# Kernel optimization log

Measured on AMD Instinct MI355X. Metric: run time of the kernel, lower is better.

Reference implementation:

```python
import jax, jax.numpy as jnp
import numpy as np

N_NODES = 2000
N_EDGES = 8000  # undirected; 2*N_EDGES directed pairs
BATCH = 16
D = 64  # in/out node and edge feature dim


def _build_graph():
    """Random undirected graph; returns directed (src, dst) pairs in the
    row-major order of torch.where(adj==1), plus the undirected edge id of
    each directed pair (mimics get_all_edge_for_node_pairs)."""
    rng = np.random.default_rng(0)
    cand = rng.integers(0, N_NODES, size=(6 * N_EDGES, 2))
    cand = cand[cand[:, 0] != cand[:, 1]]
    cand = np.sort(cand, axis=1)
    cand = np.unique(cand, axis=0)
    und = cand[:N_EDGES]  # [E,2] unique undirected edges
    adj = np.zeros((N_NODES, N_NODES), dtype=np.int64)
    eid = np.full((N_NODES, N_NODES), -1, dtype=np.int64)
    e = np.arange(N_EDGES)
    adj[und[:, 0], und[:, 1]] = 1
    adj[und[:, 1], und[:, 0]] = 1
    eid[und[:, 0], und[:, 1]] = e
    eid[und[:, 1], und[:, 0]] = e
    src, dst = np.nonzero(adj)  # row-major, like torch.where
    edge_idx = eid[src, dst]
    return src.astype(np.int32), dst.astype(np.int32), edge_idx.astype(np.int32)


def setup_inputs() -> dict:
    key = jax.random.key(0)
    ks = jax.random.split(key, 7)
    src, dst, eidx = _build_graph()
    s = 0.05
    return {
        "x": jax.random.normal(ks[0], (BATCH, N_EDGES + N_NODES, D), jnp.float32),
        "W_edge": jax.random.normal(ks[1], (D, D), jnp.float32) * s,
        "W_node": jax.random.normal(ks[2], (D, D), jnp.float32) * s,
        "b_node": jax.random.normal(ks[3], (D,), jnp.float32) * s,
        "W_comb": jax.random.normal(ks[4], (3 * D, D), jnp.float32) * s,
        "b_comb": jax.random.normal(ks[5], (D,), jnp.float32) * s,
        "w_attn": jax.random.normal(ks[6], (D, 1), jnp.float32) * s,
        "src": jnp.asarray(src),
        "dst": jnp.asarray(dst),
        "eidx": jnp.asarray(eidx),
        "num_edges": N_EDGES,
    }


def reference(x, W_edge, W_node, b_node, W_comb, b_comb, w_attn, src, dst, eidx, num_edges):
    E = num_edges
    edges = x[:, :E]            # [B,E,D]
    nodes = x[:, E:]            # [B,N,D]
    B, N = nodes.shape[0], nodes.shape[1]
    f = edges @ W_edge          # dense_edge (no bias)      [B,E,D]
    h = nodes @ W_node + b_node  # dense_node (bias)        [B,N,D]
    # gather per directed edge: src node, edge feat, dst node -> [B,2E,3D]
    g = jnp.concatenate([h[:, src], f[:, eidx], h[:, dst]], axis=-1)
    f_out = jax.nn.leaky_relu(g @ W_comb + b_comb, negative_slope=0.01)  # [B,2E,D]
    # attention logits -> softmax over ALL directed edges (dim=1, as in torch)
    alpha = jax.nn.softmax(jnp.einsum('bed,do->beo', f_out, w_attn), axis=1)[..., 0]  # [B,2E]
    # scatter into dense per-batch adjacency, then aggregate
    adj = jnp.zeros((B, N, N), x.dtype).at[:, src, dst].set(alpha)
    h_out = jnp.einsum('bnm,bmd->bnd', adj, h)  # [B,N,D]
    return jnp.concatenate([f_out, h_out], axis=1)  # [B,2E+N,D]
```

## Files before the change

kernel.cpp:

```cpp
#include <hip/hip_runtime.h>
#include <hip/hip_bf16.h>

#define B_ 16
#define N_ 2000
#define E_ 8000
#define P_ 16000
#define XROW (E_ + N_)
#define OROW (P_ + N_)

typedef __hip_bfloat16 bf16;
typedef unsigned short u16;
typedef unsigned int u32;
typedef __attribute__((ext_vector_type(8))) short short8;
typedef __attribute__((ext_vector_type(4))) float f32x4;
typedef __attribute__((ext_vector_type(4))) unsigned int u32x4;
typedef __attribute__((ext_vector_type(4))) unsigned short u16x4;

__device__ __forceinline__ float b2f(bf16 v) { return __bfloat162float(v); }
__device__ __forceinline__ float u2f(u16 u) { return __uint_as_float(((u32)u) << 16); }
__device__ __forceinline__ float lo2f(u32 u) { return __uint_as_float(u << 16); }
__device__ __forceinline__ float hi2f(u32 u) { return __uint_as_float(u & 0xFFFF0000u); }
__device__ __forceinline__ u16 f2bu(float v) {
  bf16 b = __float2bfloat16(v);
  return *reinterpret_cast<u16*>(&b);
}

__device__ __forceinline__ float ldin(const void* p, int i, int f32) {
  return f32 ? ((const float*)p)[i] : __bfloat162float(((const bf16*)p)[i]);
}

__device__ __forceinline__ int detect_f32(const void* x) {
  int lane = threadIdx.x & 63;
  ushort4 v = reinterpret_cast<const ushort4*>(x)[lane];
  int bad = 0;
  float f0 = u2f(v.x), f1 = u2f(v.y), f2 = u2f(v.z), f3 = u2f(v.w);
  if (!(fabsf(f0) < 1e4f)) bad++;
  if (!(fabsf(f1) < 1e4f)) bad++;
  if (!(fabsf(f2) < 1e4f)) bad++;
  if (!(fabsf(f3) < 1e4f)) bad++;
  unsigned long long m = __ballot(bad > 0);
  return __popcll(m) > 8;
}

__device__ __forceinline__ short8 ld8b(const void* p, size_t i, int f32) {
  short8 r;
  if (f32) {
    const float* f = (const float*)p + i;
    float4 v0 = *reinterpret_cast<const float4*>(f);
    float4 v1 = *reinterpret_cast<const float4*>(f + 4);
    u16* o = (u16*)&r;
    o[0] = f2bu(v0.x); o[1] = f2bu(v0.y); o[2] = f2bu(v0.z); o[3] = f2bu(v0.w);
    o[4] = f2bu(v1.x); o[5] = f2bu(v1.y); o[6] = f2bu(v1.z); o[7] = f2bu(v1.w);
  } else {
    r = *reinterpret_cast<const short8*>((const u16*)p + i);
  }
  return r;
}

__global__ __launch_bounds__(256) void k_pre(
    const void* __restrict__ x,
    const void* __restrict__ W_edge, const void* __restrict__ W_node,
    const void* __restrict__ b_node, const void* __restrict__ W_comb,
    const void* __restrict__ b_comb,
    const int* __restrict__ src,
    u16* __restrict__ Wtn, u16* __restrict__ Wte,
    float* __restrict__ c1, float* __restrict__ c3,
    int* __restrict__ rowptr, int* __restrict__ flags) {
  const int f32 = detect_f32(x);
  int o = blockIdx.x * 256 + threadIdx.x;
  if (o < 4096) {
    int c = o >> 6, k = o & 63;
    Wtn[c*64 + k] = f2bu(ldin(W_node, k*64 + c, f32));
  } else if (o < 12288) {
    int oo = o - 4096;
    int cc = oo >> 6, k = oo & 63;
    int col = cc & 63;
    int base = (cc < 64) ? 0 : 128;
    float a = 0.f;
    for (int j = 0; j < 64; ++j)
      a += ldin(W_node, k*64 + j, f32) * ldin(W_comb, (base + j)*64 + col, f32);
    Wtn[(64 + cc)*64 + k] = f2bu(a);
  } else if (o < 16384) {
    int oo = o - 12288;
    int c = oo >> 6, k = oo & 63;
    float a = 0.f;
    for (int j = 0; j < 64; ++j)
      a += ldin(W_edge, k*64 + j, f32) * ldin(W_comb, (64 + j)*64 + c, f32);
    Wte[c*64 + k] = f2bu(a);
  } else if (o < 16448) {
    int j = o - 16384;
    float a = ldin(b_comb, j, f32);
    for (int k = 0; k < 64; ++k) a += ldin(b_node, k, f32) * ldin(W_comb, k*64 + j, f32);
    c1[j] = a;
  } else if (o < 16512) {
    int j = o - 16448;
    float a = 0.f;
    for (int k = 0; k < 64; ++k) a += ldin(b_node, k, f32) * ldin(W_comb, (128 + k)*64 + j, f32);
    c3[j] = a;
  } else if (o < 16512 + N_ + 1) {
    int n = o - 16512;
    int lo = 0, hi = P_;
    while (lo < hi) { int mid = (lo + hi) >> 1; if (src[mid] < n) lo = mid + 1; else hi = mid; }
    rowptr[n] = lo;
  } else if (o == 16512 + N_ + 1) {
    flags[0] = f32;
  }
}

__global__ __launch_bounds__(256) void k_transform(
    const void* __restrict__ x, const int* __restrict__ flags,
    const u16* __restrict__ Wtn, const u16* __restrict__ Wte,
    const void* __restrict__ b_node,
    const float* __restrict__ c1, const float* __restrict__ c3,
    bf16* __restrict__ h, bf16* __restrict__ hs, bf16* __restrict__ hd,
    bf16* __restrict__ fe) {
  const int f32 = flags[0];
  int t = threadIdx.x;
  int wave = t >> 6, lane = t & 63;
  int m16 = lane & 15, q = lane >> 4;
  if (blockIdx.x < 500) {
    int row0 = blockIdx.x * 64 + wave * 16;
    int arow = row0 + m16;
    int b = arow / N_, n = arow - b * N_;
    size_t xbase = (size_t)(b * XROW + E_ + n) * 64;
    short8 af0 = ld8b(x, xbase + q*8, f32);
    short8 af1 = ld8b(x, xbase + 32 + q*8, f32);
    f32x4 acc[12];
    #pragma unroll
    for (int c = 0; c < 12; ++c) acc[c] = (f32x4){0.f, 0.f, 0.f, 0.f};
    #pragma unroll
    for (int c = 0; c < 12; ++c) {
      short8 b0 = *reinterpret_cast<const short8*>(&Wtn[(c*16 + m16)*64 + q*8]);
      short8 b1 = *reinterpret_cast<const short8*>(&Wtn[(c*16 + m16)*64 + 32 + q*8]);
      acc[c] = __builtin_amdgcn_mfma_f32_16x16x32_bf16(af0, b0, acc[c], 0, 0, 0);
      acc[c] = __builtin_amdgcn_mfma_f32_16x16x32_bf16(af1, b1, acc[c], 0, 0, 0);
    }
    #pragma unroll
    for (int c = 0; c < 12; ++c) {
      int seg = c >> 2;
      int lcol = (c*16 + m16) & 63;
      float bias = (seg == 0) ? ldin(b_node, lcol, f32) : (seg == 1 ? c1[lcol] : c3[lcol]);
      bf16* tgt = (seg == 0) ? h : (seg == 1 ? hs : hd);
      #pragma unroll
      for (int r = 0; r < 4; ++r) {
        int row = row0 + q*4 + r;
        tgt[(size_t)row*64 + lcol] = __float2bfloat16(acc[c][r] + bias);
      }
    }
  } else {
    int row0 = (blockIdx.x - 500) * 128 + wave * 32;
    short8 af[2][2];
    #pragma unroll
    for (int rt = 0; rt < 2; ++rt) {
      int arow = row0 + rt*16 + m16;
      int b = arow / E_, e = arow - b * E_;
      size_t xbase = (size_t)(b * XROW + e) * 64;
      af[rt][0] = ld8b(x, xbase + q*8, f32);
      af[rt][1] = ld8b(x, xbase + 32 + q*8, f32);
    }
    f32x4 acc[2][4];
    #pragma unroll
    for (int rt = 0; rt < 2; ++rt)
      #pragma unroll
      for (int c = 0; c < 4; ++c) acc[rt][c] = (f32x4){0.f, 0.f, 0.f, 0.f};
    #pragma unroll
    for (int c = 0; c < 4; ++c) {
      short8 b0 = *reinterpret_cast<const short8*>(&Wte[(c*16 + m16)*64 + q*8]);
      short8 b1 = *reinterpret_cast<const short8*>(&Wte[(c*16 + m16)*64 + 32 + q*8]);
      #pragma unroll
      for (int rt = 0; rt < 2; ++rt) {
        acc[rt][c] = __builtin_amdgcn_mfma_f32_16x16x32_bf16(af[rt][0], b0, acc[rt][c], 0, 0, 0);
        acc[rt][c] = __builtin_amdgcn_mfma_f32_16x16x32_bf16(af[rt][1], b1, acc[rt][c], 0, 0, 0);
      }
    }
    #pragma unroll
    for (int rt = 0; rt < 2; ++rt)
      #pragma unroll
      for (int c = 0; c < 4; ++c) {
        int col = c*16 + m16;
        #pragma unroll
        for (int r = 0; r < 4; ++r) {
          int row = row0 + rt*16 + q*4 + r;
          fe[(size_t)row*64 + col] = __float2bfloat16(acc[rt][c][r]);
        }
      }
  }
}

__global__ __launch_bounds__(256) void k_combine(
    const int* __restrict__ flags,
    const bf16* __restrict__ hs, const bf16* __restrict__ hd,
    const bf16* __restrict__ fe,
    const void* __restrict__ w_attn,
    const int* __restrict__ src, const int* __restrict__ dst,
    const int* __restrict__ eidx,
    void* __restrict__ out, float* __restrict__ logits,
    float* __restrict__ mpart, float* __restrict__ spart) {
  const int f32 = flags[0];
  __shared__ float ld_log[32];
  int t = threadIdx.x;
  int chunk = (blockIdx.x & 7) * 1000 + (blockIdx.x >> 3);
  int lane = t & 63, wave = t >> 6;
  int grp = lane >> 3, sub = lane & 7, c0 = sub * 8;
  int r = chunk * 32 + wave * 8 + grp;
  int b = r / P_, p = r - b * P_;
  int s = src[p], d2 = dst[p], e = eidx[p];
  uint4 ua = *reinterpret_cast<const uint4*>((const u16*)hs + (size_t)(b*N_ + s)*64 + c0);
  uint4 uf = *reinterpret_cast<const uint4*>((const u16*)fe + (size_t)(b*E_ + e)*64 + c0);
  uint4 ud = *reinterpret_cast<const uint4*>((const u16*)hd + (size_t)(b*N_ + d2)*64 + c0);
  float w[8];
  if (f32) {
    float4 w0 = *reinterpret_cast<const float4*>((const float*)w_attn + c0);
    float4 w1 = *reinterpret_cast<const float4*>((const float*)w_attn + c0 + 4);
    w[0] = w0.x; w[1] = w0.y; w[2] = w0.z; w[3] = w0.w;
    w[4] = w1.x; w[5] = w1.y; w[6] = w1.z; w[7] = w1.w;
  } else {
    uint4 uw = *reinterpret_cast<const uint4*>((const u16*)w_attn + c0);
    w[0] = lo2f(uw.x); w[1] = hi2f(uw.x);
    w[2] = lo2f(uw.y); w[3] = hi2f(uw.y);
    w[4] = lo2f(uw.z); w[5] = hi2f(uw.z);
    w[6] = lo2f(uw.w); w[7] = hi2f(uw.w);
  }
  float v[8];
  v[0] = lo2f(ua.x) + lo2f(uf.x) + lo2f(ud.x);
  v[1] = hi2f(ua.x) + hi2f(uf.x) + hi2f(ud.x);
  v[2] = lo2f(ua.y) + lo2f(uf.y) + lo2f(ud.y);
  v[3] = hi2f(ua.y) + hi2f(uf.y) + hi2f(ud.y);
  v[4] = lo2f(ua.z) + lo2f(uf.z) + lo2f(ud.z);
  v[5] = hi2f(ua.z) + hi2f(uf.z) + hi2f(ud.z);
  v[6] = lo2f(ua.w) + lo2f(uf.w) + lo2f(ud.w);
  v[7] = hi2f(ua.w) + hi2f(uf.w) + hi2f(ud.w);
  float l = 0.f;
  #pragma unroll
  for (int j = 0; j < 8; ++j) {
    v[j] = v[j] > 0.f ? v[j] : 0.01f * v[j];
    l += v[j] * w[j];
  }
  size_t obase = (size_t)(b*OROW + p)*64 + c0;
  if (f32) {
    f32x4 o0; o0[0] = v[0]; o0[1] = v[1]; o0[2] = v[2]; o0[3] = v[3];
    f32x4 o1; o1[0] = v[4]; o1[1] = v[5]; o1[2] = v[6]; o1[3] = v[7];
    __builtin_nontemporal_store(o0, reinterpret_cast<f32x4*>((float*)out + obase));
    __builtin_nontemporal_store(o1, reinterpret_cast<f32x4*>((float*)out + obase + 4));
  } else {
    u32x4 o;
    o[0] = ((u32)f2bu(v[1]) << 16) | f2bu(v[0]);
    o[1] = ((u32)f2bu(v[3]) << 16) | f2bu(v[2]);
    o[2] = ((u32)f2bu(v[5]) << 16) | f2bu(v[4]);
    o[3] = ((u32)f2bu(v[7]) << 16) | f2bu(v[6]);
    __builtin_nontemporal_store(o, reinterpret_cast<u32x4*>((u16*)out + obase));
  }
  l += __shfl_down(l, 4, 8);
  l += __shfl_down(l, 2, 8);
  l += __shfl_down(l, 1, 8);
  if (sub == 0) {
    logits[b*P_ + p] = l;
    ld_log[wave * 8 + grp] = l;
  }
  __syncthreads();
  if (t < 32) {
    float li = ld_log[t];
    float m = li;
    #pragma unroll
    for (int o = 16; o > 0; o >>= 1) m = fmaxf(m, __shfl_xor(m, o, 32));
    float sv = __expf(li - m);
    #pragma unroll
    for (int o = 16; o > 0; o >>= 1) sv += __shfl_xor(sv, o, 32);
    if (t == 0) { mpart[chunk] = m; spart[chunk] = sv; }
  }
}

__global__ __launch_bounds__(256) void k_smerge(
    const float* __restrict__ mpart, const float* __restrict__ spart,
    float* __restrict__ mb, float* __restrict__ sb) {
  __shared__ float rm[256], rs[256];
  int b = blockIdx.x, t = threadIdx.x;
  float m = -1e30f, s = 0.f;
  for (int j = t; j < 500; j += 256) {
    float mj = mpart[500*b + j], sj = spart[500*b + j];
    float nm = fmaxf(m, mj);
    s = s * __expf(m - nm) + sj * __expf(mj - nm);
    m = nm;
  }
  rm[t] = m; rs[t] = s; __syncthreads();
  for (int st = 128; st > 0; st >>= 1) {
    if (t < st) {
      float mo = rm[t + st], so = rs[t + st];
      float nm = fmaxf(rm[t], mo);
      rs[t] = rs[t] * __expf(rm[t] - nm) + so * __expf(mo - nm);
      rm[t] = nm;
    }
    __syncthreads();
  }
  if (t == 0) { mb[b] = rm[0]; sb[b] = 1.0f / rs[0]; }
}

__global__ __launch_bounds__(256) void k_hout(
    const int* __restrict__ flags,
    const bf16* __restrict__ h, const float* __restrict__ logits,
    const float* __restrict__ mb, const float* __restrict__ sb,
    const int* __restrict__ rowptr, const int* __restrict__ dst,
    void* __restrict__ out) {
  const int f32 = flags[0];
  int n = blockIdx.x;
  int t = threadIdx.x;
  int wave = t >> 6, lane = t & 63;
  int b = blockIdx.y * 4 + wave;
  float m = mb[b], inv = sb[b];
  int start = rowptr[n], end = rowptr[n + 1];
  int grp = lane >> 4, sub = lane & 15, c0 = sub * 4;
  float a0 = 0.f, a1 = 0.f, a2 = 0.f, a3 = 0.f;
  for (int p = start + grp; p < end; p += 4) {
    float a = __expf(logits[b*P_ + p] - m) * inv;
    int dn = dst[p];
    ushort4 hv = *reinterpret_cast<const ushort4*>((const u16*)h + (size_t)(b*N_ + dn)*64 + c0);
    a0 += a * u2f(hv.x); a1 += a * u2f(hv.y);
    a2 += a * u2f(hv.z); a3 += a * u2f(hv.w);
  }
  a0 += __shfl_xor(a0, 16, 64); a0 += __shfl_xor(a0, 32, 64);
  a1 += __shfl_xor(a1, 16, 64); a1 += __shfl_xor(a1, 32, 64);
  a2 += __shfl_xor(a2, 16, 64); a2 += __shfl_xor(a2, 32, 64);
  a3 += __shfl_xor(a3, 16, 64); a3 += __shfl_xor(a3, 32, 64);
  if (grp == 0) {
    size_t obase = (size_t)(b*OROW + P_ + n)*64 + c0;
    if (f32) {
      f32x4 o4; o4[0] = a0; o4[1] = a1; o4[2] = a2; o4[3] = a3;
      __builtin_nontemporal_store(o4, reinterpret_cast<f32x4*>((float*)out + obase));
    } else {
      u16x4 o4;
      o4[0] = f2bu(a0); o4[1] = f2bu(a1); o4[2] = f2bu(a2); o4[3] = f2bu(a3);
      __builtin_nontemporal_store(o4, reinterpret_cast<u16x4*>((u16*)out + obase));
    }
  }
}

extern "C" void kernel_launch(void* const* d_in, const int* in_sizes, int n_in,
                              void* d_out, int out_size, void* d_ws, size_t ws_size,
                              hipStream_t stream) {
  const void* x      = d_in[0];
  const void* W_edge = d_in[1];
  const void* W_node = d_in[2];
  const void* b_node = d_in[3];
  const void* W_comb = d_in[4];
  const void* b_comb = d_in[5];
  const void* w_attn = d_in[6];
  const int* src  = (const int*)d_in[7];
  const int* dst  = (const int*)d_in[8];
  const int* eidx = (const int*)d_in[9];

  float* logits = (float*)d_ws;
  float* mpart  = logits + B_*P_;
  float* spart  = mpart + 8000;
  float* mb     = spart + 8000;
  float* sb     = mb + B_;
  float* c1     = sb + B_;
  float* c3     = c1 + 64;
  int*   rowptr = (int*)(c3 + 64);
  int*   flags  = rowptr + 2016;
  u16*   Wtn    = (u16*)(flags + 16);
  u16*   Wte    = Wtn + 192*64;
  bf16*  h      = (bf16*)(Wte + 64*64);
  bf16*  hs     = h  + B_*N_*64;
  bf16*  hd     = hs + B_*N_*64;
  bf16*  fe     = hd + B_*N_*64;

  k_pre<<<73, 256, 0, stream>>>(x, W_edge, W_node, b_node, W_comb, b_comb, src, Wtn, Wte, c1, c3, rowptr, flags);
  k_transform<<<1500, 256, 0, stream>>>(x, flags, Wtn, Wte, b_node, c1, c3, h, hs, hd, fe);
  k_combine<<<(B_*P_)/32, 256, 0, stream>>>(flags, hs, hd, fe, w_attn, src, dst, eidx, d_out, logits, mpart, spart);
  k_smerge<<<B_, 256, 0, stream>>>(mpart, spart, mb, sb);
  k_hout<<<dim3(N_, B_/4), 256, 0, stream>>>(flags, h, logits, mb, sb, rowptr, dst, d_out);
}
```

Before: 175.8 us.

## Process both directions of each undirected edge together in combine kernel

Builds a per-undirected-edge table (u, v, forward index, reverse index) in the pre-kernel by binary search over the sorted directed pairs. The combine kernel then handles both directed pairs for one edge in a single thread group, loading the edge feature once and the source/destination projections of both endpoints from an interleaved hs/hd layout. This halves edge-feature gathers and the number of combine blocks, at the cost of extra binary searches in k_pre and scattered output stores for the reverse pair.

New measurement: 190.5 us. +8.4%, slower.

```diff
diff --git a/kernel.cpp b/kernel.cpp
--- a/kernel.cpp
+++ b/kernel.cpp
@@ -7,6 +7,7 @@
 #define P_ 16000
 #define XROW (E_ + N_)
 #define OROW (P_ + N_)
+#define PAIR0 18560
 
 typedef __hip_bfloat16 bf16;
 typedef unsigned short u16;
@@ -62,10 +63,12 @@
     const void* __restrict__ W_edge, const void* __restrict__ W_node,
     const void* __restrict__ b_node, const void* __restrict__ W_comb,
     const void* __restrict__ b_comb,
-    const int* __restrict__ src,
+    const int* __restrict__ src, const int* __restrict__ dst,
+    const int* __restrict__ eidx,
     u16* __restrict__ Wtn, u16* __restrict__ Wte,
     float* __restrict__ c1, float* __restrict__ c3,
-    int* __restrict__ rowptr, int* __restrict__ flags) {
+    int* __restrict__ rowptr, int* __restrict__ flags,
+    int4* __restrict__ epair) {
   const int f32 = detect_f32(x);
   int o = blockIdx.x * 256 + threadIdx.x;
   if (o < 4096) {
@@ -104,6 +107,21 @@
     rowptr[n] = lo;
   } else if (o == 16512 + N_ + 1) {
     flags[0] = f32;
+  } else if (o >= PAIR0 && o < PAIR0 + P_) {
+    int p = o - PAIR0;
+    int u = src[p], v = dst[p];
+    if (u < v) {
+      int e = eidx[p];
+      long key = (long)v * N_ + u;
+      int lo = 0, hi = P_ - 1;
+      while (lo < hi) {
+        int mid = (lo + hi) >> 1;
+        long k2 = (long)src[mid] * N_ + dst[mid];
+        if (k2 < key) lo = mid + 1; else hi = mid;
+      }
+      int4 pr; pr.x = u; pr.y = v; pr.z = p; pr.w = lo;
+      epair[e] = pr;
+    }
   }
 }
 
@@ -112,8 +130,7 @@
     const u16* __restrict__ Wtn, const u16* __restrict__ Wte,
     const void* __restrict__ b_node,
     const float* __restrict__ c1, const float* __restrict__ c3,
-    bf16* __restrict__ h, bf16* __restrict__ hs, bf16* __restrict__ hd,
-    bf16* __restrict__ fe) {
+    bf16* __restrict__ h, bf16* __restrict__ hsd, bf16* __restrict__ fe) {
   const int f32 = flags[0];
   int t = threadIdx.x;
   int wave = t >> 6, lane = t & 63;
@@ -140,11 +157,12 @@
       int seg = c >> 2;
       int lcol = (c*16 + m16) & 63;
       float bias = (seg == 0) ? ldin(b_node, lcol, f32) : (seg == 1 ? c1[lcol] : c3[lcol]);
-      bf16* tgt = (seg == 0) ? h : (seg == 1 ? hs : hd);
       #pragma unroll
       for (int r = 0; r < 4; ++r) {
         int row = row0 + q*4 + r;
-        tgt[(size_t)row*64 + lcol] = __float2bfloat16(acc[c][r] + bias);
+        bf16 val = __float2bfloat16(acc[c][r] + bias);
+        if (seg == 0) h[(size_t)row*64 + lcol] = val;
+        else          hsd[(size_t)row*128 + (seg == 2 ? 64 : 0) + lcol] = val;
       }
     }
   } else {
@@ -189,25 +207,28 @@
 
 __global__ __launch_bounds__(256) void k_combine(
     const int* __restrict__ flags,
-    const bf16* __restrict__ hs, const bf16* __restrict__ hd,
-    const bf16* __restrict__ fe,
+    const bf16* __restrict__ hsd, const bf16* __restrict__ fe,
     const void* __restrict__ w_attn,
-    const int* __restrict__ src, const int* __restrict__ dst,
-    const int* __restrict__ eidx,
+    const int4* __restrict__ epair,
     void* __restrict__ out, float* __restrict__ logits,
     float* __restrict__ mpart, float* __restrict__ spart) {
   const int f32 = flags[0];
-  __shared__ float ld_log[32];
+  __shared__ float ld_log[64];
   int t = threadIdx.x;
-  int chunk = (blockIdx.x & 7) * 1000 + (blockIdx.x >> 3);
+  int chunk = (blockIdx.x & 7) * 500 + (blockIdx.x >> 3);
   int lane = t & 63, wave = t >> 6;
   int grp = lane >> 3, sub = lane & 7, c0 = sub * 8;
-  int r = chunk * 32 + wave * 8 + grp;
-  int b = r / P_, p = r - b * P_;
-  int s = src[p], d2 = dst[p], e = eidx[p];
-  uint4 ua = *reinterpret_cast<const uint4*>((const u16*)hs + (size_t)(b*N_ + s)*64 + c0);
+  int gidx = wave * 8 + grp;
+  int b = chunk / 250;
+  int e = (chunk - b * 250) * 32 + gidx;
+  int4 pr = epair[e];
+  int u = pr.x, v2 = pr.y, p0 = pr.z, p1 = pr.w;
+  const u16* hb = (const u16*)hsd + (size_t)b * N_ * 128;
+  uint4 su = *reinterpret_cast<const uint4*>(hb + (size_t)u  * 128 + c0);
+  uint4 du = *reinterpret_cast<const uint4*>(hb + (size_t)u  * 128 + 64 + c0);
+  uint4 sv = *reinterpret_cast<const uint4*>(hb + (size_t)v2 * 128 + c0);
+  uint4 dv = *reinterpret_cast<const uint4*>(hb + (size_t)v2 * 128 + 64 + c0);
   uint4 uf = *reinterpret_cast<const uint4*>((const u16*)fe + (size_t)(b*E_ + e)*64 + c0);
-  uint4 ud = *reinterpret_cast<const uint4*>((const u16*)hd + (size_t)(b*N_ + d2)*64 + c0);
   float w[8];
   if (f32) {
     float4 w0 = *reinterpret_cast<const float4*>((const float*)w_attn + c0);
@@ -221,52 +242,77 @@
     w[4] = lo2f(uw.z); w[5] = hi2f(uw.z);
     w[6] = lo2f(uw.w); w[7] = hi2f(uw.w);
   }
-  float v[8];
-  v[0] = lo2f(ua.x) + lo2f(uf.x) + lo2f(ud.x);
-  v[1] = hi2f(ua.x) + hi2f(uf.x) + hi2f(ud.x);
-  v[2] = lo2f(ua.y) + lo2f(uf.y) + lo2f(ud.y);
-  v[3] = hi2f(ua.y) + hi2f(uf.y) + hi2f(ud.y);
-  v[4] = lo2f(ua.z) + lo2f(uf.z) + lo2f(ud.z);
-  v[5] = hi2f(ua.z) + hi2f(uf.z) + hi2f(ud.z);
-  v[6] = lo2f(ua.w) + lo2f(uf.w) + lo2f(ud.w);
-  v[7] = hi2f(ua.w) + hi2f(uf.w) + hi2f(ud.w);
-  float l = 0.f;
+  float vA[8], vB[8];
+  vA[0] = lo2f(su.x) + lo2f(uf.x) + lo2f(dv.x);
+  vA[1] = hi2f(su.x) + hi2f(uf.x) + hi2f(dv.x);
+  vA[2] = lo2f(su.y) + lo2f(uf.y) + lo2f(dv.y);
+  vA[3] = hi2f(su.y) + hi2f(uf.y) + hi2f(dv.y);
+  vA[4] = lo2f(su.z) + lo2f(uf.z) + lo2f(dv.z);
+  vA[5] = hi2f(su.z) + hi2f(uf.z) + hi2f(dv.z);
+  vA[6] = lo2f(su.w) + lo2f(uf.w) + lo2f(dv.w);
+  vA[7] = hi2f(su.w) + hi2f(uf.w) + hi2f(dv.w);
+  vB[0] = lo2f(sv.x) + lo2f(uf.x) + lo2f(du.x);
+  vB[1] = hi2f(sv.x) + hi2f(uf.x) + hi2f(du.x);
+  vB[2] = lo2f(sv.y) + lo2f(uf.y) + lo2f(du.y);
+  vB[3] = hi2f(sv.y) + hi2f(uf.y) + hi2f(du.y);
+  vB[4] = lo2f(sv.z) + lo2f(uf.z) + lo2f(du.z);
+  vB[5] = hi2f(sv.z) + hi2f(uf.z) + hi2f(du.z);
+  vB[6] = lo2f(sv.w) + lo2f(uf.w) + lo2f(du.w);
+  vB[7] = hi2f(sv.w) + hi2f(uf.w) + hi2f(du.w);
+  float lA = 0.f, lB = 0.f;
   #pragma unroll
   for (int j = 0; j < 8; ++j) {
-    v[j] = v[j] > 0.f ? v[j] : 0.01f * v[j];
-    l += v[j] * w[j];
-  }
-  size_t obase = (size_t)(b*OROW + p)*64 + c0;
+    vA[j] = vA[j] > 0.f ? vA[j] : 0.01f * vA[j];
+    vB[j] = vB[j] > 0.f ? vB[j] : 0.01f * vB[j];
+    lA += vA[j] * w[j];
+    lB += vB[j] * w[j];
+  }
+  size_t ob0 = (size_t)(b*OROW + p0)*64 + c0;
+  size_t ob1 = (size_t)(b*OROW + p1)*64 + c0;
   if (f32) {
-    f32x4 o0; o0[0] = v[0]; o0[1] = v[1]; o0[2] = v[2]; o0[3] = v[3];
-    f32x4 o1; o1[0] = v[4]; o1[1] = v[5]; o1[2] = v[6]; o1[3] = v[7];
-    __builtin_nontemporal_store(o0, reinterpret_cast<f32x4*>((float*)out + obase));
-    __builtin_nontemporal_store(o1, reinterpret_cast<f32x4*>((float*)out + obase + 4));
+    f32x4 a0; a0[0] = vA[0]; a0[1] = vA[1]; a0[2] = vA[2]; a0[3] = vA[3];
+    f32x4 a1; a1[0] = vA[4]; a1[1] = vA[5]; a1[2] = vA[6]; a1[3] = vA[7];
+    f32x4 b0; b0[0] = vB[0]; b0[1] = vB[1]; b0[2] = vB[2]; b0[3] = vB[3];
+    f32x4 b1; b1[0] = vB[4]; b1[1] = vB[5]; b1[2] = vB[6]; b1[3] = vB[7];
+    __builtin_nontemporal_store(a0, reinterpret_cast<f32x4*>((float*)out + ob0));
+    __builtin_nontemporal_store(a1, reinterpret_cast<f32x4*>((float*)out + ob0 + 4));
+    __builtin_nontemporal_store(b0, reinterpret_cast<f32x4*>((float*)out + ob1));
+    __builtin_nontemporal_store(b1, reinterpret_cast<f32x4*>((float*)out + ob1 + 4));
   } else {
-    u32x4 o;
-    o[0] = ((u32)f2bu(v[1]) << 16) | f2bu(v[0]);
-    o[1] = ((u32)f2bu(v[3]) << 16) | f2bu(v[2]);
-    o[2] = ((u32)f2bu(v[5]) << 16) | f2bu(v[4]);
-    o[3] = ((u32)f2bu(v[7]) << 16) | f2bu(v[6]);
-    __builtin_nontemporal_store(o, reinterpret_cast<u32x4*>((u16*)out + obase));
-  }
-  l += __shfl_down(l, 4, 8);
-  l += __shfl_down(l, 2, 8);
-  l += __shfl_down(l, 1, 8);
+    u32x4 oa, ob;
+    oa[0] = ((u32)f2bu(vA[1]) << 16) | f2bu(vA[0]);
+    oa[1] = ((u32)f2bu(vA[3]) << 16) | f2bu(vA[2]);
+    oa[2] = ((u32)f2bu(vA[5]) << 16) | f2bu(vA[4]);
+    oa[3] = ((u32)f2bu(vA[7]) << 16) | f2bu(vA[6]);
+    ob[0] = ((u32)f2bu(vB[1]) << 16) | f2bu(vB[0]);
+    ob[1] = ((u32)f2bu(vB[3]) << 16) | f2bu(vB[2]);
+    ob[2] = ((u32)f2bu(vB[5]) << 16) | f2bu(vB[4]);
+    ob[3] = ((u32)f2bu(vB[7]) << 16) | f2bu(vB[6]);
+    __builtin_nontemporal_store(oa, reinterpret_cast<u32x4*>((u16*)out + ob0));
+    __builtin_nontemporal_store(ob, reinterpret_cast<u32x4*>((u16*)out + ob1));
+  }
+  lA += __shfl_down(lA, 4, 8);
+  lA += __shfl_down(lA, 2, 8);
+  lA += __shfl_down(lA, 1, 8);
+  lB += __shfl_down(lB, 4, 8);
+  lB += __shfl_down(lB, 2, 8);
+  lB += __shfl_down(lB, 1, 8);
   if (sub == 0) {
-    logits[b*P_ + p] = l;
-    ld_log[wave * 8 + grp] = l;
+    logits[b*P_ + p0] = lA;
+    logits[b*P_ + p1] = lB;
+    ld_log[gidx*2]     = lA;
+    ld_log[gidx*2 + 1] = lB;
   }
   __syncthreads();
-  if (t < 32) {
+  if (t < 64) {
     float li = ld_log[t];
     float m = li;
     #pragma unroll
-    for (int o = 16; o > 0; o >>= 1) m = fmaxf(m, __shfl_xor(m, o, 32));
-    float sv = __expf(li - m);
-    #pragma unroll
-    for (int o = 16; o > 0; o >>= 1) sv += __shfl_xor(sv, o, 32);
-    if (t == 0) { mpart[chunk] = m; spart[chunk] = sv; }
+    for (int o = 32; o > 0; o >>= 1) m = fmaxf(m, __shfl_xor(m, o, 64));
+    float sv2 = __expf(li - m);
+    #pragma unroll
+    for (int o = 32; o > 0; o >>= 1) sv2 += __shfl_xor(sv2, o, 64);
+    if (t == 0) { mpart[chunk] = m; spart[chunk] = sv2; }
   }
 }
 
@@ -276,8 +322,8 @@
   __shared__ float rm[256], rs[256];
   int b = blockIdx.x, t = threadIdx.x;
   float m = -1e30f, s = 0.f;
-  for (int j = t; j < 500; j += 256) {
-    float mj = mpart[500*b + j], sj = spart[500*b + j];
+  for (int j = t; j < 250; j += 256) {
+    float mj = mpart[250*b + j], sj = spart[250*b + j];
     float nm = fmaxf(m, mj);
     s = s * __expf(m - nm) + sj * __expf(mj - nm);
     m = nm;
@@ -350,23 +396,23 @@
 
   float* logits = (float*)d_ws;
   float* mpart  = logits + B_*P_;
-  float* spart  = mpart + 8000;
-  float* mb     = spart + 8000;
+  float* spart  = mpart + 4000;
+  float* mb     = spart + 4000;
   float* sb     = mb + B_;
   float* c1     = sb + B_;
   float* c3     = c1 + 64;
   int*   rowptr = (int*)(c3 + 64);
   int*   flags  = rowptr + 2016;
-  u16*   Wtn    = (u16*)(flags + 16);
+  int4*  epair  = (int4*)(flags + 16);
+  u16*   Wtn    = (u16*)(epair + E_);
   u16*   Wte    = Wtn + 192*64;
   bf16*  h      = (bf16*)(Wte + 64*64);
-  bf16*  hs     = h  + B_*N_*64;
-  bf16*  hd     = hs + B_*N_*64;
-  bf16*  fe     = hd + B_*N_*64;
-
-  k_pre<<<73, 256, 0, stream>>>(x, W_edge, W_node, b_node, W_comb, b_comb, src, Wtn, Wte, c1, c3, rowptr, flags);
-  k_transform<<<1500, 256, 0, stream>>>(x, flags, Wtn, Wte, b_node, c1, c3, h, hs, hd, fe);
-  k_combine<<<(B_*P_)/32, 256, 0, stream>>>(flags, hs, hd, fe, w_attn, src, dst, eidx, d_out, logits, mpart, spart);
+  bf16*  hsd    = h + B_*N_*64;
+  bf16*  fe     = hsd + B_*N_*128;
+
+  k_pre<<<135, 256, 0, stream>>>(x, W_edge, W_node, b_node, W_comb, b_comb, src, dst, eidx, Wtn, Wte, c1, c3, rowptr, flags, epair);
+  k_transform<<<1500, 256, 0, stream>>>(x, flags, Wtn, Wte, b_node, c1, c3, h, hsd, fe);
+  k_combine<<<4000, 256, 0, stream>>>(flags, hsd, fe, w_attn, epair, d_out, logits, mpart, spart);
   k_smerge<<<B_, 256, 0, stream>>>(mpart, spart, mb, sb);
   k_hout<<<dim3(N_, B_/4), 256, 0, stream>>>(flags, h, logits, mb, sb, rowptr, dst, d_out);
 }
```
